# Performance work log

Measured on AMD Instinct MI355X. Metric: run time of the kernel, lower is better.

## Reference

```python
import jax, jax.numpy as jnp
import numpy as np

S = 8192
Q_PARAM = 256
V_PARAM = 256
SCALE = 1.0 / np.sqrt(float(Q_PARAM)).astype(np.float32)


def setup_inputs() -> dict:
    key = jax.random.key(0)
    ks = jax.random.split(key, 12)
    init = lambda k, shape, fan_in: jax.random.uniform(k, shape, jnp.float32, -1.0, 1.0) / np.sqrt(float(fan_in))
    return {
        "query": jax.random.normal(ks[0], (S, Q_PARAM), jnp.float32),
        "key": jax.random.normal(ks[1], (S, Q_PARAM), jnp.float32),
        "value": jax.random.normal(ks[2], (S, V_PARAM), jnp.float32),
        "mask": jax.random.uniform(ks[3], (S, S), jnp.float32),
        "Wq": init(ks[4], (Q_PARAM, Q_PARAM), Q_PARAM),
        "bq": init(ks[5], (Q_PARAM,), Q_PARAM),
        "Wk": init(ks[6], (Q_PARAM, Q_PARAM), Q_PARAM),
        "bk": init(ks[7], (Q_PARAM,), Q_PARAM),
        "Wv": init(ks[8], (V_PARAM, V_PARAM), V_PARAM),
        "bv": init(ks[9], (V_PARAM,), V_PARAM),
        "Wo": init(ks[10], (V_PARAM, V_PARAM), V_PARAM),
        "bo": init(ks[11], (V_PARAM,), V_PARAM),
    }


def reference(query, key, value, mask, Wq, bq, Wk, bk, Wv, bv, Wo, bo):
    # torch nn.Linear: y = x @ W.T + b
    q = query @ Wq.T + bq          # [S, q]
    k = key @ Wk.T + bk            # [S, q]
    v = value @ Wv.T + bv          # [S, v]
    scores = q @ k.T               # [S, S]
    masked = scores * mask         # multiplicative mask BEFORE softmax
    h = jax.nn.softmax(masked * SCALE, axis=1)
    h = h @ v                      # [S, v]
    return h @ Wo.T + bo
```

## Files before the change

kernel.cpp:

```cpp
#include <hip/hip_runtime.h>


#define S 8192
#define NSPLIT 4
#define BM 64
#define BN 32
#define KSPLIT_LEN (S / NSPLIT)
#define NTILES (KSPLIT_LEN / BN)

typedef unsigned short ushort_t;
typedef __attribute__((ext_vector_type(8))) __bf16 bf16x8;
typedef __attribute__((ext_vector_type(4))) float f32x4;
typedef __attribute__((ext_vector_type(4))) ushort_t ushort4_t;
typedef __attribute__((ext_vector_type(8))) ushort_t ushort8_t;

typedef const __attribute__((address_space(1))) unsigned int* gas_u32;
typedef __attribute__((address_space(3))) unsigned int* las_u32;

__device__ __forceinline__ ushort_t f2bf(float f) {
  unsigned u = __builtin_bit_cast(unsigned, f);
  u += 0x7FFFu + ((u >> 16) & 1u);
  return (ushort_t)(u >> 16);
}

__device__ __forceinline__ bf16x8 pack8(f32x4 a, f32x4 b) {
  ushort8_t u;
  u[0] = f2bf(a[0]); u[1] = f2bf(a[1]); u[2] = f2bf(a[2]); u[3] = f2bf(a[3]);
  u[4] = f2bf(b[0]); u[5] = f2bf(b[1]); u[6] = f2bf(b[2]); u[7] = f2bf(b[3]);
  return __builtin_bit_cast(bf16x8, u);
}

template <int IN_BF16, int OUT_MODE>
__global__ __launch_bounds__(256) void proj_kernel(const void* __restrict__ inp,
                                                   const float* __restrict__ W,
                                                   const float* __restrict__ bias,
                                                   void* __restrict__ outp) {
  const int tid = threadIdx.x;
  const int lane = tid & 63;
  const int w = tid >> 6;
  const int lr = lane & 15, lg = lane >> 4;
  const int row0 = blockIdx.x * 64 + w * 16;
  const int col0 = blockIdx.y * 64;

  f32x4 acc[4] = {};
  const int arow = row0 + lr;
  const int kb = lg * 8;

#pragma unroll
  for (int ks = 0; ks < 8; ++ks) {
    bf16x8 a;
    if (IN_BF16) {
      a = *(const bf16x8*)((const ushort_t*)inp + (size_t)arow * 256 + ks * 32 + kb);
    } else {
      const float* ap = (const float*)inp + (size_t)arow * 256 + ks * 32 + kb;
      f32x4 a0 = *(const f32x4*)ap;
      f32x4 a1 = *(const f32x4*)(ap + 4);
      a = pack8(a0, a1);
    }
#pragma unroll
    for (int n = 0; n < 4; ++n) {
      const float* bp = W + (size_t)(col0 + 16 * n + lr) * 256 + ks * 32 + kb;
      f32x4 b0 = *(const f32x4*)bp;
      f32x4 b1 = *(const f32x4*)(bp + 4);
      bf16x8 bb = pack8(b0, b1);
      acc[n] = __builtin_amdgcn_mfma_f32_16x16x32_bf16(a, bb, acc[n], 0, 0, 0);
    }
  }

#pragma unroll
  for (int n = 0; n < 4; ++n) {
    const int col = col0 + 16 * n + lr;
    const float bv = bias[col];
    const int rbase = row0 + lg * 4;
    if (OUT_MODE == 0) {
      ushort_t* o = (ushort_t*)outp;
#pragma unroll
      for (int r = 0; r < 4; ++r)
        o[(size_t)(rbase + r) * 256 + col] = f2bf(acc[n][r] + bv);
    } else if (OUT_MODE == 1) {
      ushort4_t pk;
#pragma unroll
      for (int r = 0; r < 4; ++r) pk[r] = f2bf(acc[n][r] + bv);
      *(ushort4_t*)((ushort_t*)outp + (size_t)col * S + rbase) = pk;
    } else {
      float* o = (float*)outp;
#pragma unroll
      for (int r = 0; r < 4; ++r)
        o[(size_t)(rbase + r) * 256 + col] = acc[n][r] + bv;
    }
  }
}

__global__ __launch_bounds__(256) void flash_kernel(
    const ushort_t* __restrict__ qb, const ushort_t* __restrict__ kbm,
    const ushort_t* __restrict__ vtb, const float* __restrict__ mask,
    float* __restrict__ Opart, float* __restrict__ lpart) {
  __shared__ __align__(16) ushort_t kt[BN * 256];
  __shared__ __align__(16) ushort_t vt[256 * BN];
  __shared__ __align__(16) ushort_t pb[4][16 * BN];

  const int tid = threadIdx.x;
  const int lane = tid & 63;
  const int w = tid >> 6;
  const int lr = lane & 15, lg = lane >> 4;
  const int split = blockIdx.y;
  const int kvbase = split * KSPLIT_LEN;
  const int qrow0 = blockIdx.x * BM + w * 16;

  bf16x8 qf[8];
#pragma unroll
  for (int ks = 0; ks < 8; ++ks)
    qf[ks] = *(const bf16x8*)(qb + (size_t)(qrow0 + lr) * 256 + ks * 32 + lg * 8);

  const float* mrow[4];
#pragma unroll
  for (int r = 0; r < 4; ++r)
    mrow[r] = mask + (size_t)(qrow0 + lg * 4 + r) * S + lr;

  f32x4 oacc[16] = {};
  float lsum[4] = {0.f, 0.f, 0.f, 0.f};

  const int pa_off = lr * (BN * 2) + lg * 16;
  const int vt_swz = ((lg ^ (lane & 3)) << 4);
  ushort_t* pbw = &pb[w][0];

#pragma unroll 1
  for (int t = 0; t < NTILES; ++t) {
    const int kv0 = kvbase + t * BN;

#pragma unroll
    for (int it = 0; it < 4; ++it) {
      int chunk = it * 256 + (w << 6) + lane;
      int r = chunk >> 5;
      int c = (chunk & 31) ^ (r & 7);
      const ushort_t* src = kbm + (size_t)(kv0 + r) * 256 + c * 8;
      __builtin_amdgcn_global_load_lds((gas_u32)src,
                                       (las_u32)(kt + it * 2048 + w * 512), 16, 0, 0);
    }
#pragma unroll
    for (int it = 0; it < 4; ++it) {
      int chunk = it * 256 + (w << 6) + lane;
      int r = chunk >> 2;
      int c = (chunk & 3) ^ (r & 3);
      const ushort_t* src = vtb + (size_t)r * S + kv0 + c * 8;
      __builtin_amdgcn_global_load_lds((gas_u32)src,
                                       (las_u32)(vt + it * 2048 + w * 512), 16, 0, 0);
    }
    __syncthreads();

    f32x4 sacc[2] = {};
#pragma unroll
    for (int ks = 0; ks < 8; ++ks) {
#pragma unroll
      for (int n = 0; n < 2; ++n) {
        int addr = ((16 * n + lr) << 9) + ((((ks << 2) + lg) ^ (lane & 7)) << 4);
        bf16x8 bk = *(const bf16x8*)((const char*)kt + addr);
        sacc[n] = __builtin_amdgcn_mfma_f32_16x16x32_bf16(qf[ks], bk, sacc[n], 0, 0, 0);
      }
    }

#pragma unroll
    for (int n = 0; n < 2; ++n) {
#pragma unroll
      for (int r = 0; r < 4; ++r) {
        float mv = __builtin_nontemporal_load(mrow[r] + kv0 + 16 * n);
        float p = exp2f(sacc[n][r] * (mv * 0.09016844005556021f));
        lsum[r] += p;
        pbw[(lg * 4 + r) * BN + 16 * n + lr] = f2bf(p);
      }
    }

    bf16x8 pa = *(const bf16x8*)((const char*)pbw + pa_off);
#pragma unroll
    for (int nd = 0; nd < 16; ++nd) {
      bf16x8 bv = *(const bf16x8*)((const char*)vt + nd * 1024 + lr * 64 + vt_swz);
      oacc[nd] = __builtin_amdgcn_mfma_f32_16x16x32_bf16(pa, bv, oacc[nd], 0, 0, 0);
    }
    __syncthreads();
  }

#pragma unroll
  for (int r = 0; r < 4; ++r) {
    float v = lsum[r];
    v += __shfl_xor(v, 1);
    v += __shfl_xor(v, 2);
    v += __shfl_xor(v, 4);
    v += __shfl_xor(v, 8);
    lsum[r] = v;
  }
  const int absrow0 = qrow0 + lg * 4;
  if (lr == 0) {
#pragma unroll
    for (int r = 0; r < 4; ++r)
      lpart[(size_t)split * S + absrow0 + r] = lsum[r];
  }
#pragma unroll
  for (int r = 0; r < 4; ++r) {
    float* orow = Opart + ((size_t)split * S + absrow0 + r) * 256 + lr;
#pragma unroll
    for (int nd = 0; nd < 16; ++nd) orow[nd * 16] = oacc[nd][r];
  }
}

__global__ __launch_bounds__(256) void combine_kernel(const float* __restrict__ Opart,
                                                      const float* __restrict__ lpart,
                                                      ushort_t* __restrict__ hb) {
  const int row = blockIdx.x;
  const int d = threadIdx.x;
  float L = 0.f, acc = 0.f;
#pragma unroll
  for (int s2 = 0; s2 < NSPLIT; ++s2) {
    L += lpart[(size_t)s2 * S + row];
    acc += Opart[((size_t)s2 * S + row) * 256 + d];
  }
  hb[(size_t)row * 256 + d] = f2bf(acc / L);
}

extern "C" void kernel_launch(void* const* d_in, const int* in_sizes, int n_in,
                              void* d_out, int out_size, void* d_ws, size_t ws_size,
                              hipStream_t stream) {
  const float* query = (const float*)d_in[0];
  const float* key   = (const float*)d_in[1];
  const float* value = (const float*)d_in[2];
  const float* mask  = (const float*)d_in[3];
  const float* Wq = (const float*)d_in[4];
  const float* bq = (const float*)d_in[5];
  const float* Wk = (const float*)d_in[6];
  const float* bk = (const float*)d_in[7];
  const float* Wv = (const float*)d_in[8];
  const float* bv = (const float*)d_in[9];
  const float* Wo = (const float*)d_in[10];
  const float* bo = (const float*)d_in[11];

  char* ws = (char*)d_ws;
  ushort_t* qb  = (ushort_t*)(ws);
  ushort_t* kb  = (ushort_t*)(ws + ((size_t)4  << 20));
  ushort_t* vtb = (ushort_t*)(ws + ((size_t)8  << 20));
  ushort_t* hb  = (ushort_t*)(ws + ((size_t)12 << 20));
  float* Opart  = (float*)(ws + ((size_t)16 << 20));
  float* lpart  = (float*)(ws + ((size_t)48 << 20));

  dim3 pgrid(S / 64, 4);
  proj_kernel<0, 0><<<pgrid, 256, 0, stream>>>(query, Wq, bq, qb);
  proj_kernel<0, 0><<<pgrid, 256, 0, stream>>>(key, Wk, bk, kb);
  proj_kernel<0, 1><<<pgrid, 256, 0, stream>>>(value, Wv, bv, vtb);

  flash_kernel<<<dim3(S / BM, NSPLIT), 256, 0, stream>>>(qb, kb, vtb, mask, Opart, lpart);

  combine_kernel<<<S, 256, 0, stream>>>(Opart, lpart, hb);

  proj_kernel<1, 2><<<pgrid, 256, 0, stream>>>(hb, Wo, bo, (float*)d_out);
}
```

Before: 263.8 us.

## Double-buffer K/V tiles and mask prefetch; pre-convert weights to bf16

The flash kernel now double-buffers the K and V tiles in LDS and prefetches the next tile's mask values into registers, so global loads overlap the current tile's MFMA work. It also switches to the hardware exp2 intrinsic. A new kernel converts all four weight matrices to bf16 once per call, so the projection kernels read bf16 weights instead of re-converting fp32 tiles in every block. The V projection now stages its transposed output through LDS to make the global stores coalesced. LDS use and register pressure rise in the flash kernel, which may lower occupancy, and the extra weight-conversion launch adds a small fixed cost.

Result: faster. 225.7 us (-14.5%).

```diff
diff --git a/kernel.cpp b/kernel.cpp
--- a/kernel.cpp
+++ b/kernel.cpp
@@ -30,63 +30,98 @@
   return __builtin_bit_cast(bf16x8, u);
 }
 
+__global__ __launch_bounds__(256) void wconv_kernel(
+    const float* __restrict__ w0, const float* __restrict__ w1,
+    const float* __restrict__ w2, const float* __restrict__ w3,
+    ushort_t* __restrict__ o0, ushort_t* __restrict__ o1,
+    ushort_t* __restrict__ o2, ushort_t* __restrict__ o3) {
+  const int m = blockIdx.y;
+  const float* w = (m == 0) ? w0 : (m == 1) ? w1 : (m == 2) ? w2 : w3;
+  ushort_t* o = (m == 0) ? o0 : (m == 1) ? o1 : (m == 2) ? o2 : o3;
+  const int idx = (blockIdx.x * 256 + threadIdx.x) * 4;
+  f32x4 v = *(const f32x4*)(w + idx);
+  ushort4_t p;
+  p[0] = f2bf(v[0]); p[1] = f2bf(v[1]); p[2] = f2bf(v[2]); p[3] = f2bf(v[3]);
+  *(ushort4_t*)(o + idx) = p;
+}
+
 template <int IN_BF16, int OUT_MODE>
 __global__ __launch_bounds__(256) void proj_kernel(const void* __restrict__ inp,
-                                                   const float* __restrict__ W,
+                                                   const ushort_t* __restrict__ Wb,
                                                    const float* __restrict__ bias,
                                                    void* __restrict__ outp) {
   const int tid = threadIdx.x;
   const int lane = tid & 63;
   const int w = tid >> 6;
   const int lr = lane & 15, lg = lane >> 4;
-  const int row0 = blockIdx.x * 64 + w * 16;
+  const int brow0 = blockIdx.x * 64;
+  const int row0 = brow0 + w * 16;
   const int col0 = blockIdx.y * 64;
 
   f32x4 acc[4] = {};
   const int arow = row0 + lr;
   const int kb = lg * 8;
 
+  bf16x8 af[8];
 #pragma unroll
   for (int ks = 0; ks < 8; ++ks) {
-    bf16x8 a;
     if (IN_BF16) {
-      a = *(const bf16x8*)((const ushort_t*)inp + (size_t)arow * 256 + ks * 32 + kb);
+      af[ks] = *(const bf16x8*)((const ushort_t*)inp + (size_t)arow * 256 + ks * 32 + kb);
     } else {
       const float* ap = (const float*)inp + (size_t)arow * 256 + ks * 32 + kb;
-      f32x4 a0 = *(const f32x4*)ap;
-      f32x4 a1 = *(const f32x4*)(ap + 4);
-      a = pack8(a0, a1);
-    }
+      af[ks] = pack8(*(const f32x4*)ap, *(const f32x4*)(ap + 4));
+    }
+  }
+
+#pragma unroll
+  for (int ks = 0; ks < 8; ++ks) {
 #pragma unroll
     for (int n = 0; n < 4; ++n) {
-      const float* bp = W + (size_t)(col0 + 16 * n + lr) * 256 + ks * 32 + kb;
-      f32x4 b0 = *(const f32x4*)bp;
-      f32x4 b1 = *(const f32x4*)(bp + 4);
-      bf16x8 bb = pack8(b0, b1);
-      acc[n] = __builtin_amdgcn_mfma_f32_16x16x32_bf16(a, bb, acc[n], 0, 0, 0);
-    }
-  }
-
-#pragma unroll
-  for (int n = 0; n < 4; ++n) {
-    const int col = col0 + 16 * n + lr;
-    const float bv = bias[col];
-    const int rbase = row0 + lg * 4;
-    if (OUT_MODE == 0) {
-      ushort_t* o = (ushort_t*)outp;
-#pragma unroll
-      for (int r = 0; r < 4; ++r)
-        o[(size_t)(rbase + r) * 256 + col] = f2bf(acc[n][r] + bv);
-    } else if (OUT_MODE == 1) {
+      bf16x8 bb = *(const bf16x8*)(Wb + (size_t)(col0 + 16 * n + lr) * 256 + ks * 32 + kb);
+      acc[n] = __builtin_amdgcn_mfma_f32_16x16x32_bf16(af[ks], bb, acc[n], 0, 0, 0);
+    }
+  }
+
+  if constexpr (OUT_MODE == 1) {
+    __shared__ __align__(16) ushort_t tb[64 * 68];
+#pragma unroll
+    for (int n = 0; n < 4; ++n) {
+      const int col = col0 + 16 * n + lr;
+      const float bv = bias[col];
+      const int cl = 16 * n + lr;
+      const int rowl = w * 16 + lg * 4;
       ushort4_t pk;
 #pragma unroll
       for (int r = 0; r < 4; ++r) pk[r] = f2bf(acc[n][r] + bv);
-      *(ushort4_t*)((ushort_t*)outp + (size_t)col * S + rbase) = pk;
-    } else {
-      float* o = (float*)outp;
-#pragma unroll
-      for (int r = 0; r < 4; ++r)
-        o[(size_t)(rbase + r) * 256 + col] = acc[n][r] + bv;
+      *(ushort4_t*)&tb[cl * 68 + rowl] = pk;
+    }
+    __syncthreads();
+    ushort_t* o = (ushort_t*)outp;
+#pragma unroll
+    for (int i = 0; i < 4; ++i) {
+      int chunk = i * 256 + tid;
+      int c = chunk >> 4;
+      int off = (chunk & 15) * 4;
+      ushort4_t v0 = *(const ushort4_t*)&tb[c * 68 + off];
+      *(ushort4_t*)(o + (size_t)(col0 + c) * S + brow0 + off) = v0;
+    }
+  } else {
+#pragma unroll
+    for (int n = 0; n < 4; ++n) {
+      const int col = col0 + 16 * n + lr;
+      const float bv = bias[col];
+      const int rbase = row0 + lg * 4;
+      if (OUT_MODE == 0) {
+        ushort_t* o = (ushort_t*)outp;
+#pragma unroll
+        for (int r = 0; r < 4; ++r)
+          o[(size_t)(rbase + r) * 256 + col] = f2bf(acc[n][r] + bv);
+      } else {
+        float* o = (float*)outp;
+#pragma unroll
+        for (int r = 0; r < 4; ++r)
+          o[(size_t)(rbase + r) * 256 + col] = acc[n][r] + bv;
+      }
     }
   }
 }
@@ -95,8 +130,8 @@
     const ushort_t* __restrict__ qb, const ushort_t* __restrict__ kbm,
     const ushort_t* __restrict__ vtb, const float* __restrict__ mask,
     float* __restrict__ Opart, float* __restrict__ lpart) {
-  __shared__ __align__(16) ushort_t kt[BN * 256];
-  __shared__ __align__(16) ushort_t vt[256 * BN];
+  __shared__ __align__(16) ushort_t kt[2 * BN * 256];
+  __shared__ __align__(16) ushort_t vt[2 * 256 * BN];
   __shared__ __align__(16) ushort_t pb[4][16 * BN];
 
   const int tid = threadIdx.x;
@@ -124,10 +159,7 @@
   const int vt_swz = ((lg ^ (lane & 3)) << 4);
   ushort_t* pbw = &pb[w][0];
 
-#pragma unroll 1
-  for (int t = 0; t < NTILES; ++t) {
-    const int kv0 = kvbase + t * BN;
-
+  auto stage = [&](int b, int kv0) {
 #pragma unroll
     for (int it = 0; it < 4; ++it) {
       int chunk = it * 256 + (w << 6) + lane;
@@ -135,7 +167,7 @@
       int c = (chunk & 31) ^ (r & 7);
       const ushort_t* src = kbm + (size_t)(kv0 + r) * 256 + c * 8;
       __builtin_amdgcn_global_load_lds((gas_u32)src,
-                                       (las_u32)(kt + it * 2048 + w * 512), 16, 0, 0);
+                                       (las_u32)(kt + b * 8192 + it * 2048 + w * 512), 16, 0, 0);
     }
 #pragma unroll
     for (int it = 0; it < 4; ++it) {
@@ -144,17 +176,40 @@
       int c = (chunk & 3) ^ (r & 3);
       const ushort_t* src = vtb + (size_t)r * S + kv0 + c * 8;
       __builtin_amdgcn_global_load_lds((gas_u32)src,
-                                       (las_u32)(vt + it * 2048 + w * 512), 16, 0, 0);
-    }
-    __syncthreads();
-
+                                       (las_u32)(vt + b * 8192 + it * 2048 + w * 512), 16, 0, 0);
+    }
+  };
+
+  stage(0, kvbase);
+  float mcur[8];
+#pragma unroll
+  for (int n = 0; n < 2; ++n)
+#pragma unroll
+    for (int r = 0; r < 4; ++r)
+      mcur[n * 4 + r] = __builtin_nontemporal_load(mrow[r] + kvbase + 16 * n);
+  __syncthreads();
+
+  for (int t = 0; t < NTILES; ++t) {
+    const int cur = t & 1;
+    const int tn = (t + 1 < NTILES) ? (t + 1) : t;
+    const int kvn = kvbase + tn * BN;
+
+    stage(cur ^ 1, kvn);
+    float mnext[8];
+#pragma unroll
+    for (int n = 0; n < 2; ++n)
+#pragma unroll
+      for (int r = 0; r < 4; ++r)
+        mnext[n * 4 + r] = __builtin_nontemporal_load(mrow[r] + kvn + 16 * n);
+
+    const char* ktc = (const char*)kt + cur * 16384;
     f32x4 sacc[2] = {};
 #pragma unroll
     for (int ks = 0; ks < 8; ++ks) {
 #pragma unroll
       for (int n = 0; n < 2; ++n) {
         int addr = ((16 * n + lr) << 9) + ((((ks << 2) + lg) ^ (lane & 7)) << 4);
-        bf16x8 bk = *(const bf16x8*)((const char*)kt + addr);
+        bf16x8 bk = *(const bf16x8*)(ktc + addr);
         sacc[n] = __builtin_amdgcn_mfma_f32_16x16x32_bf16(qf[ks], bk, sacc[n], 0, 0, 0);
       }
     }
@@ -163,19 +218,22 @@
     for (int n = 0; n < 2; ++n) {
 #pragma unroll
       for (int r = 0; r < 4; ++r) {
-        float mv = __builtin_nontemporal_load(mrow[r] + kv0 + 16 * n);
-        float p = exp2f(sacc[n][r] * (mv * 0.09016844005556021f));
+        float p = __builtin_amdgcn_exp2f(sacc[n][r] * (mcur[n * 4 + r] * 0.09016844005556021f));
         lsum[r] += p;
         pbw[(lg * 4 + r) * BN + 16 * n + lr] = f2bf(p);
       }
     }
 
+    const char* vtc = (const char*)vt + cur * 16384;
     bf16x8 pa = *(const bf16x8*)((const char*)pbw + pa_off);
 #pragma unroll
     for (int nd = 0; nd < 16; ++nd) {
-      bf16x8 bv = *(const bf16x8*)((const char*)vt + nd * 1024 + lr * 64 + vt_swz);
+      bf16x8 bv = *(const bf16x8*)(vtc + nd * 1024 + lr * 64 + vt_swz);
       oacc[nd] = __builtin_amdgcn_mfma_f32_16x16x32_bf16(pa, bv, oacc[nd], 0, 0, 0);
     }
+
+#pragma unroll
+    for (int i = 0; i < 8; ++i) mcur[i] = mnext[i];
     __syncthreads();
   }
 
@@ -239,15 +297,21 @@
   ushort_t* hb  = (ushort_t*)(ws + ((size_t)12 << 20));
   float* Opart  = (float*)(ws + ((size_t)16 << 20));
   float* lpart  = (float*)(ws + ((size_t)48 << 20));
+  ushort_t* Wqb = (ushort_t*)(ws + ((size_t)49 << 20));
+  ushort_t* Wkb = (ushort_t*)(ws + ((size_t)49 << 20) + (128u << 10));
+  ushort_t* Wvb = (ushort_t*)(ws + ((size_t)49 << 20) + (256u << 10));
+  ushort_t* Wob = (ushort_t*)(ws + ((size_t)49 << 20) + (384u << 10));
+
+  wconv_kernel<<<dim3(64, 4), 256, 0, stream>>>(Wq, Wk, Wv, Wo, Wqb, Wkb, Wvb, Wob);
 
   dim3 pgrid(S / 64, 4);
-  proj_kernel<0, 0><<<pgrid, 256, 0, stream>>>(query, Wq, bq, qb);
-  proj_kernel<0, 0><<<pgrid, 256, 0, stream>>>(key, Wk, bk, kb);
-  proj_kernel<0, 1><<<pgrid, 256, 0, stream>>>(value, Wv, bv, vtb);
+  proj_kernel<0, 0><<<pgrid, 256, 0, stream>>>(query, Wqb, bq, qb);
+  proj_kernel<0, 0><<<pgrid, 256, 0, stream>>>(key, Wkb, bk, kb);
+  proj_kernel<0, 1><<<pgrid, 256, 0, stream>>>(value, Wvb, bv, vtb);
 
   flash_kernel<<<dim3(S / BM, NSPLIT), 256, 0, stream>>>(qb, kb, vtb, mask, Opart, lpart);
 
   combine_kernel<<<S, 256, 0, stream>>>(Opart, lpart, hb);
 
-  proj_kernel<1, 2><<<pgrid, 256, 0, stream>>>(hb, Wo, bo, (float*)d_out);
-}
+  proj_kernel<1, 2><<<pgrid, 256, 0, stream>>>(hb, Wob, bo, (float*)d_out);
+}
```
